# Optimization experiments

Measured on AMD Instinct MI355X. Metric: run time of the kernel, lower is better.

Reference implementation:

```python
import jax, jax.numpy as jnp
import numpy as np

N_NODES = 100000
N_EDGES = 3200000
IN_CH = 512
HIDDEN = 64
LOC_OUT = 16
OUT_CH = 40


def setup_inputs() -> dict:
    key = jax.random.key(0)
    ks = jax.random.split(key, 10)
    return {
        "batch_x": jax.random.normal(ks[0], (N_NODES, IN_CH), dtype=jnp.float32),
        "edge_index": jax.random.randint(ks[1], (2, N_EDGES), 0, N_NODES, dtype=jnp.int64),
        "glob_emb": jax.random.normal(ks[2], (N_NODES, LOC_OUT), dtype=jnp.float32),
        "W1": jax.random.normal(ks[3], (IN_CH, HIDDEN), dtype=jnp.float32) * (1.0 / np.sqrt(IN_CH)),
        "b1": jnp.zeros((HIDDEN,), dtype=jnp.float32),
        "W2": jax.random.normal(ks[4], (HIDDEN, LOC_OUT), dtype=jnp.float32) * (1.0 / np.sqrt(HIDDEN)),
        "b2": jnp.zeros((LOC_OUT,), dtype=jnp.float32),
        "att_w1": jax.random.normal(ks[5], (LOC_OUT, 16), dtype=jnp.float32) * 0.25,
        "att_b1": jnp.zeros((16,), dtype=jnp.float32),
        "att_w2": jax.random.normal(ks[6], (16, 1), dtype=jnp.float32) * 0.25,
        "lin1_w": jax.random.normal(ks[7], (LOC_OUT, OUT_CH), dtype=jnp.float32) * 0.25,
        "lin1_b": jnp.zeros((OUT_CH,), dtype=jnp.float32),
    }


def _gcn_conv(x, W, b, row, col, n):
    # GCNConv: out = D^-1/2 (A + I) D^-1/2 (X W) + b   (PyG default: self-loops, sym norm)
    h = x @ W
    loops = jnp.arange(n, dtype=row.dtype)
    row2 = jnp.concatenate([row, loops])  # sources (x_j)
    col2 = jnp.concatenate([col, loops])  # targets (aggregation index)
    deg = jax.ops.segment_sum(jnp.ones_like(col2, dtype=h.dtype), col2, num_segments=n)
    dinv = jax.lax.rsqrt(jnp.maximum(deg, 1.0))  # deg >= 1 thanks to self-loops
    norm = dinv[row2] * dinv[col2]               # [E+N]
    agg = jax.ops.segment_sum(h[row2] * norm[:, None], col2, num_segments=n)
    return agg + b


def reference(batch_x, edge_index, glob_emb, W1, b1, W2, b2, att_w1, att_b1, att_w2, lin1_w, lin1_b):
    n = batch_x.shape[0]
    row, col = edge_index[0], edge_index[1]
    x = _gcn_conv(batch_x, W1, b1, row, col, n)
    x = jax.nn.relu(x)  # dropout p=0.0 -> identity
    x = _gcn_conv(x, W2, b2, row, col, n)  # last layer: no relu/dropout
    z = jnp.stack([x, glob_emb], axis=1)  # [N, 2, 16]
    w = jnp.tanh(z @ att_w1 + att_b1) @ att_w2  # [N, 2, 1]
    beta = jax.nn.softmax(w, axis=1)
    emb = jnp.sum(beta * z, axis=1)  # [N, 16]
    return emb @ lin1_w + lin1_b  # [N, 40]
```

## Files before the change

### kernel.cpp

```cpp
#include <hip/hip_runtime.h>

#define N_IN 512
#define HID 64
#define NBLK 256

typedef __attribute__((ext_vector_type(4))) float f32x4;
typedef __attribute__((ext_vector_type(8))) short bf16x8;

__device__ inline float bf2f(unsigned short s) {
    union { unsigned int u; float f; } v; v.u = ((unsigned int)s) << 16; return v.f;
}
__device__ inline unsigned short f2bf(float f) {
    union { float f; unsigned int u; } v; v.f = f;
    unsigned int u = v.u;
    return (unsigned short)((u + 0x7FFFu + ((u >> 16) & 1u)) >> 16);
}

__global__ __launch_bounds__(1024) void k_histA_wt(const int* __restrict__ EI, int* __restrict__ hist,
                                                   const float* __restrict__ W1, unsigned short* __restrict__ Wt,
                                                   int E, int N, int K) {
    int tid = threadIdx.x;
    if (blockIdx.x >= NBLK) {
        int i = (blockIdx.x - NBLK) * 1024 + tid;
        if (i < N_IN * HID) {
            int k = i >> 6, n = i & 63;
            Wt[n * 512 + k] = f2bf(W1[i]);
        }
        return;
    }
    __shared__ int hs[512];
    __shared__ int sflag;
    if (tid == 0) sflag = (EI[1] == 0 && EI[3] == 0 && EI[5] == 0 && EI[7] == 0) ? 1 : 0;
    if (tid < 512) hs[tid] = 0;
    __syncthreads();
    bool f = sflag != 0;
    int chunk = (E + NBLK - 1) / NBLK;
    int s = blockIdx.x * chunk, e = min(E, s + chunk);
    for (int i = s + tid; i < e; i += 1024) {
        int c = f ? ((const int2*)EI)[E + i].x : EI[E + i];
        if ((unsigned)c < (unsigned)N) atomicAdd(&hs[c >> 8], 1);
    }
    __syncthreads();
    for (int k = tid; k < K; k += 1024) hist[k * NBLK + blockIdx.x] = hs[k];
}

__global__ __launch_bounds__(256) void k_scan_a2(int* __restrict__ data, int* __restrict__ bsum, int n) {
    __shared__ int sd[256];
    int i = blockIdx.x * 256 + threadIdx.x;
    int v = (i < n) ? data[i] : 0;
    sd[threadIdx.x] = v;
    __syncthreads();
    for (int off = 1; off < 256; off <<= 1) {
        int t = 0;
        if (threadIdx.x >= (unsigned)off) t = sd[threadIdx.x - off];
        __syncthreads();
        sd[threadIdx.x] += t;
        __syncthreads();
    }
    if (i < n) data[i] = sd[threadIdx.x] - v;
    if (threadIdx.x == 255) bsum[blockIdx.x] = sd[255];
}

__global__ __launch_bounds__(512) void k_scan_b(const int* __restrict__ bsum, int* __restrict__ bexc, int nb,
                                                unsigned short* __restrict__ h1, unsigned short* __restrict__ h2,
                                                int N) {
    __shared__ int sd[512];
    int t = threadIdx.x;
    if (t < 32) ((unsigned int*)(h1 + (size_t)N * 64))[t] = 0;
    if (t >= 32 && t < 40) ((unsigned int*)(h2 + (size_t)N * 16))[t - 32] = 0;
    int v = (t < nb) ? bsum[t] : 0;
    sd[t] = v;
    __syncthreads();
    for (int off = 1; off < 512; off <<= 1) {
        int u = 0;
        if (t >= off) u = sd[t - off];
        __syncthreads();
        sd[t] += u;
        __syncthreads();
    }
    if (t < nb) bexc[t] = sd[t] - v;
    if (t == 511) bexc[nb] = sd[511];
}

__global__ __launch_bounds__(1024) void k_partB(const int* __restrict__ EI, const int* __restrict__ hist,
                                                const int* __restrict__ bexc, int* __restrict__ edges2,
                                                int E, int N, int K) {
    __shared__ int cur[512];
    __shared__ int sflag;
    int tid = threadIdx.x, b = blockIdx.x;
    if (tid == 0) sflag = (EI[1] == 0 && EI[3] == 0 && EI[5] == 0 && EI[7] == 0) ? 1 : 0;
    if (tid < 512) cur[tid] = (tid < K) ? (bexc[tid] + hist[tid * NBLK + b]) : 0;
    __syncthreads();
    bool f = sflag != 0;
    int chunk = (E + NBLK - 1) / NBLK;
    int s = b * chunk, e = min(E, s + chunk);
    for (int i = s + tid; i < e; i += 1024) {
        int r, c;
        if (f) { const int2* E2 = (const int2*)EI; r = E2[i].x; c = E2[E + i].x; }
        else   { r = EI[i]; c = EI[E + i]; }
        if ((unsigned)r >= (unsigned)N || (unsigned)c >= (unsigned)N) continue;
        int pos = atomicAdd(&cur[c >> 8], 1);
        edges2[pos] = r | ((c & 255) << 20);
    }
}

__global__ __launch_bounds__(256) void k_gemm1(const float* __restrict__ X, const unsigned short* __restrict__ Wt,
                                               unsigned short* __restrict__ H, int N) {
    int tid = threadIdx.x;
    int w = tid >> 6, lane = tid & 63;
    int m_l = lane & 15, q = lane >> 4;
    int m0 = blockIdx.x * 128 + w * 32;
    int rA0 = m0 + m_l, rA1 = m0 + 16 + m_l;
    int rc0 = rA0 < N ? rA0 : N - 1;
    int rc1 = rA1 < N ? rA1 : N - 1;
    const float* baseA0 = X + (size_t)rc0 * 512 + q * 8;
    const float* baseA1 = X + (size_t)rc1 * 512 + q * 8;
    const unsigned short* baseB = Wt + (size_t)m_l * 512 + q * 8;

    f32x4 acc[2][4] = {};
#pragma unroll 4
    for (int c = 0; c < 16; ++c) {
        int ko = c * 32;
        float4 x0a = *(const float4*)(baseA0 + ko);
        float4 x0b = *(const float4*)(baseA0 + ko + 4);
        float4 x1a = *(const float4*)(baseA1 + ko);
        float4 x1b = *(const float4*)(baseA1 + ko + 4);
        bf16x8 a0, a1;
        a0[0] = (short)f2bf(x0a.x); a0[1] = (short)f2bf(x0a.y); a0[2] = (short)f2bf(x0a.z); a0[3] = (short)f2bf(x0a.w);
        a0[4] = (short)f2bf(x0b.x); a0[5] = (short)f2bf(x0b.y); a0[6] = (short)f2bf(x0b.z); a0[7] = (short)f2bf(x0b.w);
        a1[0] = (short)f2bf(x1a.x); a1[1] = (short)f2bf(x1a.y); a1[2] = (short)f2bf(x1a.z); a1[3] = (short)f2bf(x1a.w);
        a1[4] = (short)f2bf(x1b.x); a1[5] = (short)f2bf(x1b.y); a1[6] = (short)f2bf(x1b.z); a1[7] = (short)f2bf(x1b.w);
#pragma unroll
        for (int t = 0; t < 4; ++t) {
            bf16x8 bb = *(const bf16x8*)(baseB + (size_t)t * 16 * 512 + ko);
            acc[0][t] = __builtin_amdgcn_mfma_f32_16x16x32_bf16(a0, bb, acc[0][t], 0, 0, 0);
            acc[1][t] = __builtin_amdgcn_mfma_f32_16x16x32_bf16(a1, bb, acc[1][t], 0, 0, 0);
        }
    }
#pragma unroll
    for (int h = 0; h < 2; ++h) {
#pragma unroll
        for (int rg = 0; rg < 4; ++rg) {
            int row = m0 + h * 16 + q * 4 + rg;
            if (row < N) {
#pragma unroll
                for (int t = 0; t < 4; ++t)
                    H[(size_t)row * 64 + t * 16 + m_l] = f2bf(acc[h][t][rg]);
            }
        }
    }
}

__global__ __launch_bounds__(256) void k_bucket(const int* __restrict__ bexc, const int* __restrict__ edges2,
                                                int* __restrict__ edges, int* __restrict__ start,
                                                int* __restrict__ endv, float* __restrict__ dinv,
                                                unsigned short* __restrict__ H, int N, int K) {
    __shared__ int hist[256], sd[256], cur[256];
    __shared__ float dvs[256];
    int b = blockIdx.x, tid = threadIdx.x;
    int cbase = bexc[b];
    int cend  = bexc[b + 1];
    int base  = ((cbase + 3) & ~3) + 1024 * b;
    hist[tid] = 0;
    __syncthreads();
    for (int i = cbase + tid; i < cend; i += 256)
        atomicAdd(&hist[(edges2[i] >> 20) & 255], 1);
    __syncthreads();
    int v = hist[tid];
    int v4 = (v + 3) & ~3;
    sd[tid] = v4;
    __syncthreads();
    for (int off = 1; off < 256; off <<= 1) {
        int t = 0;
        if (tid >= off) t = sd[tid - off];
        __syncthreads();
        sd[tid] += t;
        __syncthreads();
    }
    int excl = sd[tid] - v4;
    cur[tid] = excl;
    int node = b * 256 + tid;
    float dvv = rsqrtf((float)(v + 1));
    dvs[tid] = dvv;
    if (node < N) {
        start[node] = base + excl;
        endv[node]  = base + excl + v;
        dinv[node]  = dvv;
    }
    __syncthreads();
    for (int i = cbase + tid; i < cend; i += 256) {
        int pv = edges2[i];
        int pos = atomicAdd(&cur[(pv >> 20) & 255], 1);
        edges[base + pos] = pv & 0xFFFFF;
    }
    for (int rr = tid >> 4; rr < 256; rr += 16) {
        int n2 = b * 256 + rr;
        if (n2 < N) {
            float dv2 = dvs[rr];
            uint2* pp = (uint2*)(H + (size_t)n2 * 64 + (size_t)(tid & 15) * 4);
            uint2 vv = *pp;
            float f0 = bf2f((unsigned short)(vv.x & 0xffffu)) * dv2;
            float f1 = bf2f((unsigned short)(vv.x >> 16)) * dv2;
            float f2 = bf2f((unsigned short)(vv.y & 0xffffu)) * dv2;
            float f3 = bf2f((unsigned short)(vv.y >> 16)) * dv2;
            vv.x = (unsigned int)f2bf(f0) | ((unsigned int)f2bf(f1) << 16);
            vv.y = (unsigned int)f2bf(f2) | ((unsigned int)f2bf(f3) << 16);
            *pp = vv;
        }
    }
}

#define ACC8(v) do { \
    a[0] += __uint_as_float((v).x << 16); \
    a[1] += __uint_as_float((v).x & 0xffff0000u); \
    a[2] += __uint_as_float((v).y << 16); \
    a[3] += __uint_as_float((v).y & 0xffff0000u); \
    a[4] += __uint_as_float((v).z << 16); \
    a[5] += __uint_as_float((v).z & 0xffff0000u); \
    a[6] += __uint_as_float((v).w << 16); \
    a[7] += __uint_as_float((v).w & 0xffff0000u); } while (0)

__global__ __launch_bounds__(256) void k_agg1g2(const unsigned short* __restrict__ H, const int* __restrict__ edges,
                                                const int* __restrict__ start, const int* __restrict__ endv,
                                                const float* __restrict__ dinv,
                                                const float* __restrict__ b1, const float* __restrict__ W2,
                                                unsigned short* __restrict__ H2, int N) {
    __shared__ float w2s[64 * 17];
    int tid = threadIdx.x;
    for (int i = tid; i < 1024; i += 256) { int k = i >> 4, c = i & 15; w2s[k * 17 + c] = W2[i]; }
    __syncthreads();
    int wid = blockIdx.x * 4 + (tid >> 6);
    int lane = tid & 63;
    if (wid >= N) return;
    int g8 = (lane >> 3) * 8;
    int c8 = lane & 7;
    const size_t coff = (size_t)c8 * 8;
    float a[8] = {0.f, 0.f, 0.f, 0.f, 0.f, 0.f, 0.f, 0.f};
    int s = start[wid], e = endv[wid];
    int4 s0, s1;
    if (s < e) {
        s0 = *(const int4*)(edges + s + g8);
        s1 = *(const int4*)(edges + s + g8 + 4);
    }
    for (int i = s; i < e; i += 64) {
        int jb = i + g8;
        int i0 = (jb + 0 < e) ? s0.x : N;
        int i1 = (jb + 1 < e) ? s0.y : N;
        int i2 = (jb + 2 < e) ? s0.z : N;
        int i3 = (jb + 3 < e) ? s0.w : N;
        int i4 = (jb + 4 < e) ? s1.x : N;
        int i5 = (jb + 5 < e) ? s1.y : N;
        int i6 = (jb + 6 < e) ? s1.z : N;
        int i7 = (jb + 7 < e) ? s1.w : N;
        uint4 v0 = *(const uint4*)(H + (size_t)i0 * 64 + coff);
        uint4 v1 = *(const uint4*)(H + (size_t)i1 * 64 + coff);
        uint4 v2 = *(const uint4*)(H + (size_t)i2 * 64 + coff);
        uint4 v3 = *(const uint4*)(H + (size_t)i3 * 64 + coff);
        uint4 v4 = *(const uint4*)(H + (size_t)i4 * 64 + coff);
        uint4 v5 = *(const uint4*)(H + (size_t)i5 * 64 + coff);
        uint4 v6 = *(const uint4*)(H + (size_t)i6 * 64 + coff);
        uint4 v7 = *(const uint4*)(H + (size_t)i7 * 64 + coff);
        int ni = i + 64;
        if (ni < e) {
            s0 = *(const int4*)(edges + ni + g8);
            s1 = *(const int4*)(edges + ni + g8 + 4);
        }
        ACC8(v0); ACC8(v1); ACC8(v2); ACC8(v3);
        ACC8(v4); ACC8(v5); ACC8(v6); ACC8(v7);
    }
#pragma unroll
    for (int c = 0; c < 8; ++c) {
        a[c] += __shfl_xor(a[c], 8, 64);
        a[c] += __shfl_xor(a[c], 16, 64);
        a[c] += __shfl_xor(a[c], 32, 64);
    }
    float dv = dinv[wid];
    uint4 sv = *(const uint4*)(H + (size_t)wid * 64 + coff);
    ACC8(sv);
    float4 bva = *(const float4*)(b1 + c8 * 8);
    float4 bvb = *(const float4*)(b1 + c8 * 8 + 4);
    float r[8];
    r[0] = fmaxf(a[0] * dv + bva.x, 0.f);
    r[1] = fmaxf(a[1] * dv + bva.y, 0.f);
    r[2] = fmaxf(a[2] * dv + bva.z, 0.f);
    r[3] = fmaxf(a[3] * dv + bva.w, 0.f);
    r[4] = fmaxf(a[4] * dv + bvb.x, 0.f);
    r[5] = fmaxf(a[5] * dv + bvb.y, 0.f);
    r[6] = fmaxf(a[6] * dv + bvb.z, 0.f);
    r[7] = fmaxf(a[7] * dv + bvb.w, 0.f);
    int qt = lane >> 4, co = lane & 15;
    float p = 0.f;
#pragma unroll
    for (int j = 0; j < 16; ++j) {
        float xk = __shfl(r[j & 7], qt * 2 + (j >> 3), 64);
        p += xk * w2s[(qt * 16 + j) * 17 + co];
    }
    p += __shfl_xor(p, 16, 64);
    p += __shfl_xor(p, 32, 64);
    if (lane < 16) H2[(size_t)wid * 16 + co] = f2bf(p * dv);
}

__global__ __launch_bounds__(256) void k_agg2(const unsigned short* __restrict__ H2, const int* __restrict__ edges,
                                              const int* __restrict__ start, const int* __restrict__ endv,
                                              const float* __restrict__ dinv,
                                              const float* __restrict__ b2, float* __restrict__ X2, int N) {
    int wid = blockIdx.x * 4 + (threadIdx.x >> 6);
    int lane = threadIdx.x & 63;
    if (wid >= N) return;
    int g8 = (lane >> 2) * 8;
    int c4 = lane & 3;
    const size_t coff = (size_t)c4 * 4;
    float a0 = 0.f, a1 = 0.f, a2 = 0.f, a3 = 0.f;
    int s = start[wid], e = endv[wid];
    int4 s0, s1;
    if (s < e) {
        s0 = *(const int4*)(edges + s + g8);
        s1 = *(const int4*)(edges + s + g8 + 4);
    }
    for (int i = s; i < e; i += 128) {
        int jb = i + g8;
        int i0 = (jb + 0 < e) ? s0.x : N;
        int i1 = (jb + 1 < e) ? s0.y : N;
        int i2 = (jb + 2 < e) ? s0.z : N;
        int i3 = (jb + 3 < e) ? s0.w : N;
        int i4 = (jb + 4 < e) ? s1.x : N;
        int i5 = (jb + 5 < e) ? s1.y : N;
        int i6 = (jb + 6 < e) ? s1.z : N;
        int i7 = (jb + 7 < e) ? s1.w : N;
        uint2 v0 = *(const uint2*)(H2 + (size_t)i0 * 16 + coff);
        uint2 v1 = *(const uint2*)(H2 + (size_t)i1 * 16 + coff);
        uint2 v2 = *(const uint2*)(H2 + (size_t)i2 * 16 + coff);
        uint2 v3 = *(const uint2*)(H2 + (size_t)i3 * 16 + coff);
        uint2 v4 = *(const uint2*)(H2 + (size_t)i4 * 16 + coff);
        uint2 v5 = *(const uint2*)(H2 + (size_t)i5 * 16 + coff);
        uint2 v6 = *(const uint2*)(H2 + (size_t)i6 * 16 + coff);
        uint2 v7 = *(const uint2*)(H2 + (size_t)i7 * 16 + coff);
        int ni = i + 128;
        if (ni < e) {
            s0 = *(const int4*)(edges + ni + g8);
            s1 = *(const int4*)(edges + ni + g8 + 4);
        }
        a0 += __uint_as_float(v0.x << 16) + __uint_as_float(v1.x << 16)
            + __uint_as_float(v2.x << 16) + __uint_as_float(v3.x << 16)
            + __uint_as_float(v4.x << 16) + __uint_as_float(v5.x << 16)
            + __uint_as_float(v6.x << 16) + __uint_as_float(v7.x << 16);
        a1 += __uint_as_float(v0.x & 0xffff0000u) + __uint_as_float(v1.x & 0xffff0000u)
            + __uint_as_float(v2.x & 0xffff0000u) + __uint_as_float(v3.x & 0xffff0000u)
            + __uint_as_float(v4.x & 0xffff0000u) + __uint_as_float(v5.x & 0xffff0000u)
            + __uint_as_float(v6.x & 0xffff0000u) + __uint_as_float(v7.x & 0xffff0000u);
        a2 += __uint_as_float(v0.y << 16) + __uint_as_float(v1.y << 16)
            + __uint_as_float(v2.y << 16) + __uint_as_float(v3.y << 16)
            + __uint_as_float(v4.y << 16) + __uint_as_float(v5.y << 16)
            + __uint_as_float(v6.y << 16) + __uint_as_float(v7.y << 16);
        a3 += __uint_as_float(v0.y & 0xffff0000u) + __uint_as_float(v1.y & 0xffff0000u)
            + __uint_as_float(v2.y & 0xffff0000u) + __uint_as_float(v3.y & 0xffff0000u)
            + __uint_as_float(v4.y & 0xffff0000u) + __uint_as_float(v5.y & 0xffff0000u)
            + __uint_as_float(v6.y & 0xffff0000u) + __uint_as_float(v7.y & 0xffff0000u);
    }
    a0 += __shfl_xor(a0, 4, 64); a0 += __shfl_xor(a0, 8, 64); a0 += __shfl_xor(a0, 16, 64); a0 += __shfl_xor(a0, 32, 64);
    a1 += __shfl_xor(a1, 4, 64); a1 += __shfl_xor(a1, 8, 64); a1 += __shfl_xor(a1, 16, 64); a1 += __shfl_xor(a1, 32, 64);
    a2 += __shfl_xor(a2, 4, 64); a2 += __shfl_xor(a2, 8, 64); a2 += __shfl_xor(a2, 16, 64); a2 += __shfl_xor(a2, 32, 64);
    a3 += __shfl_xor(a3, 4, 64); a3 += __shfl_xor(a3, 8, 64); a3 += __shfl_xor(a3, 16, 64); a3 += __shfl_xor(a3, 32, 64);
    if (lane < 4) {
        float dv = dinv[wid];
        uint2 sv = *(const uint2*)(H2 + (size_t)wid * 16 + coff);
        a0 += __uint_as_float(sv.x << 16);
        a1 += __uint_as_float(sv.x & 0xffff0000u);
        a2 += __uint_as_float(sv.y << 16);
        a3 += __uint_as_float(sv.y & 0xffff0000u);
        float4 bv = *(const float4*)(b2 + c4 * 4);
        float4 o;
        o.x = a0 * dv + bv.x; o.y = a1 * dv + bv.y;
        o.z = a2 * dv + bv.z; o.w = a3 * dv + bv.w;
        *(float4*)(X2 + (size_t)wid * 16 + c4 * 4) = o;
    }
}

__global__ __launch_bounds__(256) void k_head(const float* __restrict__ X2, const float* __restrict__ G,
                                              const float* __restrict__ AW1, const float* __restrict__ AB1,
                                              const float* __restrict__ AW2, const float* __restrict__ LW,
                                              const float* __restrict__ LB, float* __restrict__ OUT, int N) {
    __shared__ float s_aw1[256], s_ab1[16], s_aw2[16], s_lw[640], s_lb[40];
    __shared__ float s_out[256 * 41];
    int tid = threadIdx.x;
    s_aw1[tid] = AW1[tid];
    if (tid < 16) { s_ab1[tid] = AB1[tid]; s_aw2[tid] = AW2[tid]; }
    for (int i = tid; i < 640; i += 256) s_lw[i] = LW[i];
    if (tid < 40) s_lb[tid] = LB[tid];
    __syncthreads();
    int node0 = blockIdx.x * 256;
    int node = node0 + tid;
    if (node < N) {
        float x[16], g[16];
        const float4* xp = (const float4*)(X2 + (size_t)node * 16);
        const float4* gp = (const float4*)(G + (size_t)node * 16);
#pragma unroll
        for (int q = 0; q < 4; ++q) {
            float4 v = xp[q]; x[q*4] = v.x; x[q*4+1] = v.y; x[q*4+2] = v.z; x[q*4+3] = v.w;
            float4 u = gp[q]; g[q*4] = u.x; g[q*4+1] = u.y; g[q*4+2] = u.z; g[q*4+3] = u.w;
        }
        float wx = 0.f, wg = 0.f;
#pragma unroll
        for (int j = 0; j < 16; ++j) {
            float tx = s_ab1[j], tg = s_ab1[j];
#pragma unroll
            for (int c = 0; c < 16; ++c) { tx += x[c] * s_aw1[c*16 + j]; tg += g[c] * s_aw1[c*16 + j]; }
            wx += tanhf(tx) * s_aw2[j];
            wg += tanhf(tg) * s_aw2[j];
        }
        float m = fmaxf(wx, wg);
        float ex = expf(wx - m), eg = expf(wg - m);
        float inv = 1.f / (ex + eg);
        float bx = ex * inv, bg = eg * inv;
        float emb[16];
#pragma unroll
        for (int c = 0; c < 16; ++c) emb[c] = bx * x[c] + bg * g[c];
        for (int o = 0; o < 40; ++o) {
            float a = s_lb[o];
#pragma unroll
            for (int c = 0; c < 16; ++c) a += emb[c] * s_lw[c*40 + o];
            s_out[tid * 41 + o] = a;
        }
    }
    __syncthreads();
    int lim = min(256, N - node0) * 40;
    for (int i = tid; i < lim; i += 256) {
        int r = i / 40, c = i - r * 40;
        OUT[(size_t)node0 * 40 + i] = s_out[r * 41 + c];
    }
}

extern "C" void kernel_launch(void* const* d_in, const int* in_sizes, int n_in,
                              void* d_out, int out_size, void* d_ws, size_t ws_size,
                              hipStream_t stream) {
    const float* X   = (const float*)d_in[0];
    const int*   EI  = (const int*)d_in[1];
    const float* G   = (const float*)d_in[2];
    const float* W1  = (const float*)d_in[3];
    const float* B1  = (const float*)d_in[4];
    const float* W2  = (const float*)d_in[5];
    const float* B2  = (const float*)d_in[6];
    const float* AW1 = (const float*)d_in[7];
    const float* AB1 = (const float*)d_in[8];
    const float* AW2 = (const float*)d_in[9];
    const float* LW  = (const float*)d_in[10];
    const float* LB  = (const float*)d_in[11];
    float* OUT = (float*)d_out;

    const int N = in_sizes[0] / N_IN;
    const int E = in_sizes[1] / 2;
    const int NB = (N + 255) / 256;
    const int K  = NB;
    const int NH = K * NBLK;
    const int SB = (NH + 255) / 256;
    const int WB = (N_IN * HID + 1023) / 1024;
    const int GB = (N + 127) / 128;

    char* w = (char*)d_ws;
    size_t off = 0;
    auto take = [&](size_t bytes) -> void* {
        void* p = (void*)(w + off);
        off = (off + bytes + 255) & ~(size_t)255;
        return p;
    };
    int*   hist   = (int*)take((size_t)NH * 4);
    int*   bsum   = (int*)take((size_t)SB * 4);
    int*   bexc   = (int*)take((size_t)(SB + 1) * 4);
    int*   startp = (int*)take((size_t)N * 4);
    int*   endp   = (int*)take((size_t)N * 4);
    float* dinvp  = (float*)take((size_t)N * 4);
    int*   edges2 = (int*)take((size_t)E * 4);
    int*   edges  = (int*)take((size_t)(E + 1024 * (size_t)K + 256) * 4);
    unsigned short* wt = (unsigned short*)take((size_t)N_IN * HID * 2);
    unsigned short* h1 = (unsigned short*)take((size_t)(N + 1) * 64 * 2);
    unsigned short* h2 = (unsigned short*)take((size_t)(N + 1) * 16 * 2);
    float* x2 = (float*)take((size_t)N * 16 * 4);
    (void)ws_size; (void)n_in; (void)out_size;

    k_histA_wt<<<NBLK + WB, 1024, 0, stream>>>(EI, hist, W1, wt, E, N, K);
    k_scan_a2 <<<SB, 256, 0, stream>>>(hist, bsum, NH);
    k_scan_b  <<<1, 512, 0, stream>>>(bsum, bexc, SB, h1, h2, N);
    k_partB   <<<NBLK, 1024, 0, stream>>>(EI, hist, bexc, edges2, E, N, K);
    k_gemm1   <<<GB, 256, 0, stream>>>(X, wt, h1, N);
    k_bucket  <<<K, 256, 0, stream>>>(bexc, edges2, edges, startp, endp, dinvp, h1, N, K);
    k_agg1g2  <<<(N + 3) / 4, 256, 0, stream>>>(h1, edges, startp, endp, dinvp, B1, W2, h2, N);
    k_agg2    <<<(N + 3) / 4, 256, 0, stream>>>(h2, edges, startp, endp, dinvp, B2, x2, N);
    k_head    <<<NB, 256, 0, stream>>>(x2, G, AW1, AB1, AW2, LW, LB, OUT, N);
}
```

Baseline: 555.7 us.

## Fold dinv scaling into GEMM epilogue, narrow gather loops, drop head LDS staging

Moves k_bucket ahead of the GEMM so the GEMM epilogue can apply the dinv row scaling directly. This removes the extra read-modify-write pass over H inside k_bucket. Both aggregation kernels now gather 4 neighbours per lane-group per iteration instead of 8, and k_agg2 uses 8 lanes of 2 channels each. The head kernel writes output rows directly instead of staging them in shared memory for coalesced stores. The trade-offs are less memory-level parallelism in the gathers and strided uncoalesced output stores in the head.

```diff
diff --git a/kernel.cpp b/kernel.cpp
--- a/kernel.cpp
+++ b/kernel.cpp
@@ -104,8 +104,50 @@
     }
 }
 
+__global__ __launch_bounds__(256) void k_bucket(const int* __restrict__ bexc, const int* __restrict__ edges2,
+                                                int* __restrict__ edges, int* __restrict__ start,
+                                                int* __restrict__ endv, float* __restrict__ dinv,
+                                                int N, int K) {
+    __shared__ int hist[256], sd[256], cur[256];
+    int b = blockIdx.x, tid = threadIdx.x;
+    int cbase = bexc[b];
+    int cend  = bexc[b + 1];
+    int base  = ((cbase + 3) & ~3) + 1024 * b;
+    hist[tid] = 0;
+    __syncthreads();
+    for (int i = cbase + tid; i < cend; i += 256)
+        atomicAdd(&hist[(edges2[i] >> 20) & 255], 1);
+    __syncthreads();
+    int v = hist[tid];
+    int v4 = (v + 3) & ~3;
+    sd[tid] = v4;
+    __syncthreads();
+    for (int off = 1; off < 256; off <<= 1) {
+        int t = 0;
+        if (tid >= off) t = sd[tid - off];
+        __syncthreads();
+        sd[tid] += t;
+        __syncthreads();
+    }
+    int excl = sd[tid] - v4;
+    cur[tid] = excl;
+    int node = b * 256 + tid;
+    if (node < N) {
+        start[node] = base + excl;
+        endv[node]  = base + excl + v;
+        dinv[node]  = rsqrtf((float)(v + 1));
+    }
+    __syncthreads();
+    for (int i = cbase + tid; i < cend; i += 256) {
+        int pv = edges2[i];
+        int pos = atomicAdd(&cur[(pv >> 20) & 255], 1);
+        edges[base + pos] = pv & 0xFFFFF;
+    }
+}
+
 __global__ __launch_bounds__(256) void k_gemm1(const float* __restrict__ X, const unsigned short* __restrict__ Wt,
-                                               unsigned short* __restrict__ H, int N) {
+                                               const float* __restrict__ dinv, unsigned short* __restrict__ H,
+                                               int N) {
     int tid = threadIdx.x;
     int w = tid >> 6, lane = tid & 63;
     int m_l = lane & 15, q = lane >> 4;
@@ -143,69 +185,11 @@
         for (int rg = 0; rg < 4; ++rg) {
             int row = m0 + h * 16 + q * 4 + rg;
             if (row < N) {
+                float dv = dinv[row];
 #pragma unroll
                 for (int t = 0; t < 4; ++t)
-                    H[(size_t)row * 64 + t * 16 + m_l] = f2bf(acc[h][t][rg]);
+                    H[(size_t)row * 64 + t * 16 + m_l] = f2bf(acc[h][t][rg] * dv);
             }
-        }
-    }
-}
-
-__global__ __launch_bounds__(256) void k_bucket(const int* __restrict__ bexc, const int* __restrict__ edges2,
-                                                int* __restrict__ edges, int* __restrict__ start,
-                                                int* __restrict__ endv, float* __restrict__ dinv,
-                                                unsigned short* __restrict__ H, int N, int K) {
-    __shared__ int hist[256], sd[256], cur[256];
-    __shared__ float dvs[256];
-    int b = blockIdx.x, tid = threadIdx.x;
-    int cbase = bexc[b];
-    int cend  = bexc[b + 1];
-    int base  = ((cbase + 3) & ~3) + 1024 * b;
-    hist[tid] = 0;
-    __syncthreads();
-    for (int i = cbase + tid; i < cend; i += 256)
-        atomicAdd(&hist[(edges2[i] >> 20) & 255], 1);
-    __syncthreads();
-    int v = hist[tid];
-    int v4 = (v + 3) & ~3;
-    sd[tid] = v4;
-    __syncthreads();
-    for (int off = 1; off < 256; off <<= 1) {
-        int t = 0;
-        if (tid >= off) t = sd[tid - off];
-        __syncthreads();
-        sd[tid] += t;
-        __syncthreads();
-    }
-    int excl = sd[tid] - v4;
-    cur[tid] = excl;
-    int node = b * 256 + tid;
-    float dvv = rsqrtf((float)(v + 1));
-    dvs[tid] = dvv;
-    if (node < N) {
-        start[node] = base + excl;
-        endv[node]  = base + excl + v;
-        dinv[node]  = dvv;
-    }
-    __syncthreads();
-    for (int i = cbase + tid; i < cend; i += 256) {
-        int pv = edges2[i];
-        int pos = atomicAdd(&cur[(pv >> 20) & 255], 1);
-        edges[base + pos] = pv & 0xFFFFF;
-    }
-    for (int rr = tid >> 4; rr < 256; rr += 16) {
-        int n2 = b * 256 + rr;
-        if (n2 < N) {
-            float dv2 = dvs[rr];
-            uint2* pp = (uint2*)(H + (size_t)n2 * 64 + (size_t)(tid & 15) * 4);
-            uint2 vv = *pp;
-            float f0 = bf2f((unsigned short)(vv.x & 0xffffu)) * dv2;
-            float f1 = bf2f((unsigned short)(vv.x >> 16)) * dv2;
-            float f2 = bf2f((unsigned short)(vv.y & 0xffffu)) * dv2;
-            float f3 = bf2f((unsigned short)(vv.y >> 16)) * dv2;
-            vv.x = (unsigned int)f2bf(f0) | ((unsigned int)f2bf(f1) << 16);
-            vv.y = (unsigned int)f2bf(f2) | ((unsigned int)f2bf(f3) << 16);
-            *pp = vv;
         }
     }
 }
@@ -232,41 +216,26 @@
     int wid = blockIdx.x * 4 + (tid >> 6);
     int lane = tid & 63;
     if (wid >= N) return;
-    int g8 = (lane >> 3) * 8;
+    int sg4 = (lane >> 3) * 4;
     int c8 = lane & 7;
     const size_t coff = (size_t)c8 * 8;
     float a[8] = {0.f, 0.f, 0.f, 0.f, 0.f, 0.f, 0.f, 0.f};
     int s = start[wid], e = endv[wid];
-    int4 s0, s1;
-    if (s < e) {
-        s0 = *(const int4*)(edges + s + g8);
-        s1 = *(const int4*)(edges + s + g8 + 4);
-    }
-    for (int i = s; i < e; i += 64) {
-        int jb = i + g8;
+    int4 s0;
+    if (s < e) s0 = *(const int4*)(edges + s + sg4);
+    for (int i = s; i < e; i += 32) {
+        int jb = i + sg4;
         int i0 = (jb + 0 < e) ? s0.x : N;
         int i1 = (jb + 1 < e) ? s0.y : N;
         int i2 = (jb + 2 < e) ? s0.z : N;
         int i3 = (jb + 3 < e) ? s0.w : N;
-        int i4 = (jb + 4 < e) ? s1.x : N;
-        int i5 = (jb + 5 < e) ? s1.y : N;
-        int i6 = (jb + 6 < e) ? s1.z : N;
-        int i7 = (jb + 7 < e) ? s1.w : N;
         uint4 v0 = *(const uint4*)(H + (size_t)i0 * 64 + coff);
         uint4 v1 = *(const uint4*)(H + (size_t)i1 * 64 + coff);
         uint4 v2 = *(const uint4*)(H + (size_t)i2 * 64 + coff);
         uint4 v3 = *(const uint4*)(H + (size_t)i3 * 64 + coff);
-        uint4 v4 = *(const uint4*)(H + (size_t)i4 * 64 + coff);
-        uint4 v5 = *(const uint4*)(H + (size_t)i5 * 64 + coff);
-        uint4 v6 = *(const uint4*)(H + (size_t)i6 * 64 + coff);
-        uint4 v7 = *(const uint4*)(H + (size_t)i7 * 64 + coff);
-        int ni = i + 64;
-        if (ni < e) {
-            s0 = *(const int4*)(edges + ni + g8);
-            s1 = *(const int4*)(edges + ni + g8 + 4);
-        }
+        int ni = i + 32;
+        if (ni < e) s0 = *(const int4*)(edges + ni + sg4);
         ACC8(v0); ACC8(v1); ACC8(v2); ACC8(v3);
-        ACC8(v4); ACC8(v5); ACC8(v6); ACC8(v7);
     }
 #pragma unroll
     for (int c = 0; c < 8; ++c) {
@@ -307,72 +276,40 @@
     int wid = blockIdx.x * 4 + (threadIdx.x >> 6);
     int lane = threadIdx.x & 63;
     if (wid >= N) return;
-    int g8 = (lane >> 2) * 8;
-    int c4 = lane & 3;
-    const size_t coff = (size_t)c4 * 4;
-    float a0 = 0.f, a1 = 0.f, a2 = 0.f, a3 = 0.f;
+    int sg4 = (lane >> 3) * 4;
+    int c2 = lane & 7;
+    const size_t coff = (size_t)c2 * 2;
+    float a0 = 0.f, a1 = 0.f;
     int s = start[wid], e = endv[wid];
-    int4 s0, s1;
-    if (s < e) {
-        s0 = *(const int4*)(edges + s + g8);
-        s1 = *(const int4*)(edges + s + g8 + 4);
-    }
-    for (int i = s; i < e; i += 128) {
-        int jb = i + g8;
+    int4 s0;
+    if (s < e) s0 = *(const int4*)(edges + s + sg4);
+    for (int i = s; i < e; i += 32) {
+        int jb = i + sg4;
         int i0 = (jb + 0 < e) ? s0.x : N;
         int i1 = (jb + 1 < e) ? s0.y : N;
         int i2 = (jb + 2 < e) ? s0.z : N;
         int i3 = (jb + 3 < e) ? s0.w : N;
-        int i4 = (jb + 4 < e) ? s1.x : N;
-        int i5 = (jb + 5 < e) ? s1.y : N;
-        int i6 = (jb + 6 < e) ? s1.z : N;
-        int i7 = (jb + 7 < e) ? s1.w : N;
-        uint2 v0 = *(const uint2*)(H2 + (size_t)i0 * 16 + coff);
-        uint2 v1 = *(const uint2*)(H2 + (size_t)i1 * 16 + coff);
-        uint2 v2 = *(const uint2*)(H2 + (size_t)i2 * 16 + coff);
-        uint2 v3 = *(const uint2*)(H2 + (size_t)i3 * 16 + coff);
-        uint2 v4 = *(const uint2*)(H2 + (size_t)i4 * 16 + coff);
-        uint2 v5 = *(const uint2*)(H2 + (size_t)i5 * 16 + coff);
-        uint2 v6 = *(const uint2*)(H2 + (size_t)i6 * 16 + coff);
-        uint2 v7 = *(const uint2*)(H2 + (size_t)i7 * 16 + coff);
-        int ni = i + 128;
-        if (ni < e) {
-            s0 = *(const int4*)(edges + ni + g8);
-            s1 = *(const int4*)(edges + ni + g8 + 4);
-        }
-        a0 += __uint_as_float(v0.x << 16) + __uint_as_float(v1.x << 16)
-            + __uint_as_float(v2.x << 16) + __uint_as_float(v3.x << 16)
-            + __uint_as_float(v4.x << 16) + __uint_as_float(v5.x << 16)
-            + __uint_as_float(v6.x << 16) + __uint_as_float(v7.x << 16);
-        a1 += __uint_as_float(v0.x & 0xffff0000u) + __uint_as_float(v1.x & 0xffff0000u)
-            + __uint_as_float(v2.x & 0xffff0000u) + __uint_as_float(v3.x & 0xffff0000u)
-            + __uint_as_float(v4.x & 0xffff0000u) + __uint_as_float(v5.x & 0xffff0000u)
-            + __uint_as_float(v6.x & 0xffff0000u) + __uint_as_float(v7.x & 0xffff0000u);
-        a2 += __uint_as_float(v0.y << 16) + __uint_as_float(v1.y << 16)
-            + __uint_as_float(v2.y << 16) + __uint_as_float(v3.y << 16)
-            + __uint_as_float(v4.y << 16) + __uint_as_float(v5.y << 16)
-            + __uint_as_float(v6.y << 16) + __uint_as_float(v7.y << 16);
-        a3 += __uint_as_float(v0.y & 0xffff0000u) + __uint_as_float(v1.y & 0xffff0000u)
-            + __uint_as_float(v2.y & 0xffff0000u) + __uint_as_float(v3.y & 0xffff0000u)
-            + __uint_as_float(v4.y & 0xffff0000u) + __uint_as_float(v5.y & 0xffff0000u)
-            + __uint_as_float(v6.y & 0xffff0000u) + __uint_as_float(v7.y & 0xffff0000u);
-    }
-    a0 += __shfl_xor(a0, 4, 64); a0 += __shfl_xor(a0, 8, 64); a0 += __shfl_xor(a0, 16, 64); a0 += __shfl_xor(a0, 32, 64);
-    a1 += __shfl_xor(a1, 4, 64); a1 += __shfl_xor(a1, 8, 64); a1 += __shfl_xor(a1, 16, 64); a1 += __shfl_xor(a1, 32, 64);
-    a2 += __shfl_xor(a2, 4, 64); a2 += __shfl_xor(a2, 8, 64); a2 += __shfl_xor(a2, 16, 64); a2 += __shfl_xor(a2, 32, 64);
-    a3 += __shfl_xor(a3, 4, 64); a3 += __shfl_xor(a3, 8, 64); a3 += __shfl_xor(a3, 16, 64); a3 += __shfl_xor(a3, 32, 64);
-    if (lane < 4) {
+        unsigned int v0 = *(const unsigned int*)(H2 + (size_t)i0 * 16 + coff);
+        unsigned int v1 = *(const unsigned int*)(H2 + (size_t)i1 * 16 + coff);
+        unsigned int v2 = *(const unsigned int*)(H2 + (size_t)i2 * 16 + coff);
+        unsigned int v3 = *(const unsigned int*)(H2 + (size_t)i3 * 16 + coff);
+        int ni = i + 32;
+        if (ni < e) s0 = *(const int4*)(edges + ni + sg4);
+        a0 += __uint_as_float(v0 << 16) + __uint_as_float(v1 << 16)
+            + __uint_as_float(v2 << 16) + __uint_as_float(v3 << 16);
+        a1 += __uint_as_float(v0 & 0xffff0000u) + __uint_as_float(v1 & 0xffff0000u)
+            + __uint_as_float(v2 & 0xffff0000u) + __uint_as_float(v3 & 0xffff0000u);
+    }
+    a0 += __shfl_xor(a0, 8, 64); a0 += __shfl_xor(a0, 16, 64); a0 += __shfl_xor(a0, 32, 64);
+    a1 += __shfl_xor(a1, 8, 64); a1 += __shfl_xor(a1, 16, 64); a1 += __shfl_xor(a1, 32, 64);
+    if (lane < 8) {
         float dv = dinv[wid];
-        uint2 sv = *(const uint2*)(H2 + (size_t)wid * 16 + coff);
-        a0 += __uint_as_float(sv.x << 16);
-        a1 += __uint_as_float(sv.x & 0xffff0000u);
-        a2 += __uint_as_float(sv.y << 16);
-        a3 += __uint_as_float(sv.y & 0xffff0000u);
-        float4 bv = *(const float4*)(b2 + c4 * 4);
-        float4 o;
-        o.x = a0 * dv + bv.x; o.y = a1 * dv + bv.y;
-        o.z = a2 * dv + bv.z; o.w = a3 * dv + bv.w;
-        *(float4*)(X2 + (size_t)wid * 16 + c4 * 4) = o;
+        unsigned int sv = *(const unsigned int*)(H2 + (size_t)wid * 16 + coff);
+        a0 += __uint_as_float(sv << 16);
+        a1 += __uint_as_float(sv & 0xffff0000u);
+        float2 bv = *(const float2*)(b2 + c2 * 2);
+        float2 o; o.x = a0 * dv + bv.x; o.y = a1 * dv + bv.y;
+        *(float2*)(X2 + (size_t)wid * 16 + coff) = o;
     }
 }
 
@@ -381,52 +318,44 @@
                                               const float* __restrict__ AW2, const float* __restrict__ LW,
                                               const float* __restrict__ LB, float* __restrict__ OUT, int N) {
     __shared__ float s_aw1[256], s_ab1[16], s_aw2[16], s_lw[640], s_lb[40];
-    __shared__ float s_out[256 * 41];
     int tid = threadIdx.x;
     s_aw1[tid] = AW1[tid];
     if (tid < 16) { s_ab1[tid] = AB1[tid]; s_aw2[tid] = AW2[tid]; }
     for (int i = tid; i < 640; i += 256) s_lw[i] = LW[i];
     if (tid < 40) s_lb[tid] = LB[tid];
     __syncthreads();
-    int node0 = blockIdx.x * 256;
-    int node = node0 + tid;
-    if (node < N) {
-        float x[16], g[16];
-        const float4* xp = (const float4*)(X2 + (size_t)node * 16);
-        const float4* gp = (const float4*)(G + (size_t)node * 16);
-#pragma unroll
-        for (int q = 0; q < 4; ++q) {
-            float4 v = xp[q]; x[q*4] = v.x; x[q*4+1] = v.y; x[q*4+2] = v.z; x[q*4+3] = v.w;
-            float4 u = gp[q]; g[q*4] = u.x; g[q*4+1] = u.y; g[q*4+2] = u.z; g[q*4+3] = u.w;
-        }
-        float wx = 0.f, wg = 0.f;
-#pragma unroll
-        for (int j = 0; j < 16; ++j) {
-            float tx = s_ab1[j], tg = s_ab1[j];
-#pragma unroll
-            for (int c = 0; c < 16; ++c) { tx += x[c] * s_aw1[c*16 + j]; tg += g[c] * s_aw1[c*16 + j]; }
-            wx += tanhf(tx) * s_aw2[j];
-            wg += tanhf(tg) * s_aw2[j];
-        }
-        float m = fmaxf(wx, wg);
-        float ex = expf(wx - m), eg = expf(wg - m);
-        float inv = 1.f / (ex + eg);
-        float bx = ex * inv, bg = eg * inv;
-        float emb[16];
-#pragma unroll
-        for (int c = 0; c < 16; ++c) emb[c] = bx * x[c] + bg * g[c];
-        for (int o = 0; o < 40; ++o) {
-            float a = s_lb[o];
-#pragma unroll
-            for (int c = 0; c < 16; ++c) a += emb[c] * s_lw[c*40 + o];
-            s_out[tid * 41 + o] = a;
-        }
-    }
-    __syncthreads();
-    int lim = min(256, N - node0) * 40;
-    for (int i = tid; i < lim; i += 256) {
-        int r = i / 40, c = i - r * 40;
-        OUT[(size_t)node0 * 40 + i] = s_out[r * 41 + c];
+    int node = blockIdx.x * 256 + tid;
+    if (node >= N) return;
+    float x[16], g[16];
+    const float4* xp = (const float4*)(X2 + (size_t)node * 16);
+    const float4* gp = (const float4*)(G + (size_t)node * 16);
+#pragma unroll
+    for (int q = 0; q < 4; ++q) {
+        float4 v = xp[q]; x[q*4] = v.x; x[q*4+1] = v.y; x[q*4+2] = v.z; x[q*4+3] = v.w;
+        float4 u = gp[q]; g[q*4] = u.x; g[q*4+1] = u.y; g[q*4+2] = u.z; g[q*4+3] = u.w;
+    }
+    float wx = 0.f, wg = 0.f;
+#pragma unroll
+    for (int j = 0; j < 16; ++j) {
+        float tx = s_ab1[j], tg = s_ab1[j];
+#pragma unroll
+        for (int c = 0; c < 16; ++c) { tx += x[c] * s_aw1[c*16 + j]; tg += g[c] * s_aw1[c*16 + j]; }
+        wx += tanhf(tx) * s_aw2[j];
+        wg += tanhf(tg) * s_aw2[j];
+    }
+    float m = fmaxf(wx, wg);
+    float ex = expf(wx - m), eg = expf(wg - m);
+    float inv = 1.f / (ex + eg);
+    float bx = ex * inv, bg = eg * inv;
+    float emb[16];
+#pragma unroll
+    for (int c = 0; c < 16; ++c) emb[c] = bx * x[c] + bg * g[c];
+    float* op = OUT + (size_t)node * 40;
+    for (int o = 0; o < 40; ++o) {
+        float a = s_lb[o];
+#pragma unroll
+        for (int c = 0; c < 16; ++c) a += emb[c] * s_lw[c*40 + o];
+        op[o] = a;
     }
 }
 
@@ -481,8 +410,8 @@
     k_scan_a2 <<<SB, 256, 0, stream>>>(hist, bsum, NH);
     k_scan_b  <<<1, 512, 0, stream>>>(bsum, bexc, SB, h1, h2, N);
     k_partB   <<<NBLK, 1024, 0, stream>>>(EI, hist, bexc, edges2, E, N, K);
-    k_gemm1   <<<GB, 256, 0, stream>>>(X, wt, h1, N);
-    k_bucket  <<<K, 256, 0, stream>>>(bexc, edges2, edges, startp, endp, dinvp, h1, N, K);
+    k_bucket  <<<K, 256, 0, stream>>>(bexc, edges2, edges, startp, endp, dinvp, N, K);
+    k_gemm1   <<<GB, 256, 0, stream>>>(X, wt, dinvp, h1, N);
     k_agg1g2  <<<(N + 3) / 4, 256, 0, stream>>>(h1, edges, startp, endp, dinvp, B1, W2, h2, N);
     k_agg2    <<<(N + 3) / 4, 256, 0, stream>>>(h2, edges, startp, endp, dinvp, B2, x2, N);
     k_head    <<<NB, 256, 0, stream>>>(x2, G, AW1, AB1, AW2, LW, LB, OUT, N);
```

Result: faster. 527.1 us (-5.1%).
